# Kernel tuning notes

Hardware: AMD Instinct MI355X
Metric: run time of the kernel (lower is better)

The kernel has to match this reference:

```python
import jax, jax.numpy as jnp
import numpy as np

B, C, H, W = 16, 1536, 32, 32
M = 64      # num_clusters
L = 128     # cluster_dim
G = 256     # token_dim
HID = 512
OT_ITERS = 3
EPS = 1e-6


def setup_inputs() -> dict:
    key = jax.random.key(0)
    ks = jax.random.split(key, 12)
    def w(k, shape, fan_in):
        return jax.random.normal(k, shape, jnp.float32) * (1.0 / np.sqrt(fan_in))
    return {
        'x': jax.random.normal(ks[0], (B, C, H, W), jnp.float32),
        't': jax.random.normal(ks[1], (B, C), jnp.float32),
        # token_features: Linear(C->512), ReLU, Linear(512->G)
        'Wt1': w(ks[2], (HID, C), C), 'bt1': jnp.zeros((HID,), jnp.float32),
        'Wt2': w(ks[3], (G, HID), HID), 'bt2': jnp.zeros((G,), jnp.float32),
        # cluster_features: 1x1 Conv(C->512), ReLU, 1x1 Conv(512->L)
        'Wc1': w(ks[4], (HID, C), C), 'bc1': jnp.zeros((HID,), jnp.float32),
        'Wc2': w(ks[5], (L, HID), HID), 'bc2': jnp.zeros((L,), jnp.float32),
        # score: 1x1 Conv(C->512), ReLU, 1x1 Conv(512->M)
        'Ws1': w(ks[6], (HID, C), C), 'bs1': jnp.zeros((HID,), jnp.float32),
        'Ws2': w(ks[7], (M, HID), HID), 'bs2': jnp.zeros((M,), jnp.float32),
        # temp_predictor: Conv1d(L->1, k=1)
        'Wtp': w(ks[8], (L,), L), 'btp': jnp.zeros((), jnp.float32),
        'dust_bin': jnp.asarray(1.0, jnp.float32),
        'burst_b': jnp.asarray(0.0, jnp.float32),
        'burst_p': jnp.asarray(1.0, jnp.float32),
        'lambda_discount': jnp.asarray(0.5, jnp.float32),
    }


def _log_optimal_transport(scores, alpha, iters):
    # scores: [B, m, n]; alpha: scalar dust-bin logit
    b, m, n = scores.shape
    Z0 = jnp.concatenate([scores, jnp.broadcast_to(alpha, (b, 1, n))], axis=1)  # [B, m+1, n]
    norm = -jnp.log(jnp.asarray(m + n, scores.dtype))
    log_mu = jnp.concatenate([jnp.full((m,), norm, scores.dtype),
                              (jnp.log(jnp.asarray(n, scores.dtype)) + norm)[None]])  # [m+1]
    log_nu = jnp.full((n,), norm, scores.dtype)
    u = jnp.zeros((b, m + 1), scores.dtype)
    v = jnp.zeros((b, n), scores.dtype)
    for _ in range(iters):
        u = log_mu - jax.nn.logsumexp(Z0 + v[:, None, :], axis=2)
        v = log_nu - jax.nn.logsumexp(Z0 + u[:, :, None], axis=1)
    return Z0 + u[:, :, None] + v[:, None, :] - norm


def _l2norm(a, axis):
    return a / jnp.maximum(jnp.linalg.norm(a, axis=axis, keepdims=True), 1e-12)


def _forward(x, t, Wt1, bt1, Wt2, bt2, Wc1, bc1, Wc2, bc2, Ws1, bs1, Ws2, bs2,
             Wtp, btp, dust_bin, burst_b, burst_p, lambda_discount):
    b, c, h, w = x.shape
    n = h * w
    xf = x.reshape(b, c, n)  # [B, C, N] (1x1 convs == per-pixel MLP)
    # cluster features f: [B, L, N]
    h1 = jax.nn.relu(jnp.einsum('bcn,oc->bon', xf, Wc1) + bc1[:, None])
    f = jnp.einsum('bhn,lh->bln', h1, Wc2) + bc2[:, None]
    # assignment scores p: [B, M, N]
    h2 = jax.nn.relu(jnp.einsum('bcn,oc->bon', xf, Ws1) + bs1[:, None])
    p = jnp.einsum('bhn,mh->bmn', h2, Ws2) + bs2[:, None]
    # global token: [B, G]
    tok = jax.nn.relu(t @ Wt1.T + bt1) @ Wt2.T + bt2
    # Sinkhorn OT soft assignment, drop dust bin row
    P = jnp.exp(_log_optimal_transport(p, dust_bin, OT_ITERS))[:, :-1, :]  # [B, M, N]
    # burst-aware weighting
    f_norm = _l2norm(f, axis=1)                                  # [B, L, N]
    T_i = jax.nn.softplus(jnp.einsum('bln,l->bn', f, Wtp) + btp)  # [B, N]
    sim = jnp.einsum('bli,blj->bij', f_norm, f_norm)              # [B, N, N]
    T_avg = (T_i[:, :, None] + T_i[:, None, :]) * 0.5
    burst_w = jax.nn.sigmoid(T_avg * sim + burst_b)
    discount = jnp.clip(jnp.sum(burst_w, axis=-1) ** burst_p, 1e-3, 1e3)  # [B, N]
    lam = jax.nn.sigmoid(lambda_discount)
    P_adj = (1.0 - lam) * P + lam * (P / (discount[:, None, :] + EPS))
    # local aggregation: (f[:, :, None, :] * P[:, None, :, :]).sum(-1) == batched matmul
    agg = jnp.einsum('bln,bmn->blm', f, P_adj)  # [B, L, M]
    agg = _l2norm(agg, axis=1).reshape(b, -1)   # [B, L*M]
    tok_n = _l2norm(tok, axis=-1)
    g = jnp.concatenate([tok_n, agg], axis=-1)  # [B, G + L*M]
    return _l2norm(g, axis=-1)


def reference(x, t, Wt1, bt1, Wt2, bt2, Wc1, bc1, Wc2, bc2, Ws1, bs1, Ws2, bs2,
              Wtp, btp, dust_bin, burst_b, burst_p, lambda_discount):
    return _forward(x, t, Wt1, bt1, Wt2, bt2, Wc1, bc1, Wc2, bc2, Ws1, bs1, Ws2, bs2,
                    Wtp, btp, dust_bin, burst_b, burst_p, lambda_discount)
```

## Files before the change

kernel.cpp:

```cpp
#include <hip/hip_runtime.h>
#include <math.h>

#define B_   16
#define C_   1536
#define N_   1024
#define M_   64
#define L_   128
#define G_   256
#define HID_ 512

typedef __attribute__((ext_vector_type(8))) short short8;
typedef __attribute__((ext_vector_type(4))) float floatx4;

__device__ __forceinline__ unsigned short f2bf_rne(float x) {
    unsigned u = __float_as_uint(x);
    unsigned r = u + 0x7fffu + ((u >> 16) & 1u);
    return (unsigned short)(r >> 16);
}
__device__ __forceinline__ unsigned pack_bf2(float lo, float hi) {
    unsigned a = __float_as_uint(lo) + 0x8000u;
    unsigned b = __float_as_uint(hi) + 0x8000u;
    return (a >> 16) | (b & 0xffff0000u);
}

__device__ __forceinline__ void gl2lds16(const void* g, void* l) {
    __builtin_amdgcn_global_load_lds(
        (const __attribute__((address_space(1))) void*)g,
        (__attribute__((address_space(3))) void*)l, 16, 0, 0);
}

__global__ __launch_bounds__(256) void cast_w_kernel(
    const float* __restrict__ Wc1, const float* __restrict__ Ws1,
    const float* __restrict__ Wc2, const float* __restrict__ Ws2,
    unsigned short* __restrict__ Wbf, unsigned short* __restrict__ W2)
{
    const int T1 = 1024 * 1536;
    int idx = blockIdx.x * 256 + threadIdx.x;
    if (idx < T1) {
        float v = (idx < 512 * 1536) ? Wc1[idx] : Ws1[idx - 512 * 1536];
        Wbf[idx] = f2bf_rne(v);
    } else if (idx < T1 + 192 * 1024) {
        int i2 = idx - T1;
        int row = i2 >> 10, k = i2 & 1023;
        float v = 0.f;
        if (row < 128) { if (k < 512) v = Wc2[row * 512 + k]; }
        else           { if (k >= 512) v = Ws2[(row - 128) * 512 + (k - 512)]; }
        W2[i2] = f2bf_rne(v);
    }
}

__global__ __launch_bounds__(256) void xt_kernel(
    const float* __restrict__ x, unsigned short* __restrict__ xT)
{
    __shared__ float Xs[64][65];
    const int t = threadIdx.x;
    const int n0 = blockIdx.x * 64, c0 = blockIdx.y * 64, b = blockIdx.z;
    const float* xb = x + (long)b * C_ * N_;
    #pragma unroll
    for (int it = 0; it < 16; ++it) {
        int idx = it * 256 + t, cr = idx >> 6, nc = idx & 63;
        Xs[cr][nc] = xb[(long)(c0 + cr) * N_ + n0 + nc];
    }
    __syncthreads();
    unsigned* xo = (unsigned*)(xT + (long)b * N_ * C_);
    #pragma unroll
    for (int it = 0; it < 8; ++it) {
        int idx = it * 256 + t, nr = idx >> 5, pc = idx & 31;
        xo[(long)(n0 + nr) * 768 + (c0 >> 1) + pc] =
            pack_bf2(Xs[2 * pc][nr], Xs[2 * pc + 1][nr]);
    }
}

__global__ __launch_bounds__(256, 2) void gemm1_kernel(
    const unsigned short* __restrict__ Wbf, const unsigned short* __restrict__ xT,
    const float* __restrict__ bc1, const float* __restrict__ bs1,
    unsigned short* __restrict__ hT)
{
    __shared__ unsigned short As[128 * 32];
    __shared__ unsigned short Bs[128 * 32];
    const int t = threadIdx.x;
    const int lane = t & 63, w = t >> 6;
    const int n0 = blockIdx.x * 128, o0 = blockIdx.y * 128, b = blockIdx.z;
    const unsigned short* xb = xT + (long)b * N_ * C_;

    const int wo = (w >> 1) * 64, wn = (w & 1) * 64;
    const int lrow = lane & 15, kgrp = lane >> 4;
    const int arow = t >> 2, acol = (t & 3) * 8;

    floatx4 acc[4][4];
    #pragma unroll
    for (int i = 0; i < 4; ++i)
        #pragma unroll
        for (int j = 0; j < 4; ++j) acc[i][j] = (floatx4)0.0f;

    for (int k0 = 0; k0 < C_; k0 += 32) {
        #pragma unroll
        for (int r = 0; r < 2; ++r)
            gl2lds16(Wbf + (long)(o0 + r * 64 + arow) * C_ + k0 + acol,
                     (char*)As + r * 4096 + t * 16);
        #pragma unroll
        for (int r = 0; r < 2; ++r)
            gl2lds16(xb + (long)(n0 + r * 64 + arow) * C_ + k0 + acol,
                     (char*)Bs + r * 4096 + t * 16);
        __syncthreads();
        short8 af[4], bfr[4];
        #pragma unroll
        for (int i = 0; i < 4; ++i)
            af[i] = *(const short8*)((const char*)As +
                        (wo + i * 16 + lrow) * 64 + kgrp * 16);
        #pragma unroll
        for (int j = 0; j < 4; ++j)
            bfr[j] = *(const short8*)((const char*)Bs +
                        (wn + j * 16 + lrow) * 64 + kgrp * 16);
        #pragma unroll
        for (int i = 0; i < 4; ++i)
            #pragma unroll
            for (int j = 0; j < 4; ++j)
                acc[i][j] = __builtin_amdgcn_mfma_f32_16x16x32_bf16(
                    af[i], bfr[j], acc[i][j], 0, 0, 0);
        __syncthreads();
    }

    const float* bias = (o0 < 512) ? bc1 : bs1;
    const int ob = (o0 < 512) ? o0 : o0 - 512;
    #pragma unroll
    for (int i = 0; i < 4; ++i) {
        int orow = wo + i * 16 + kgrp * 4;
        float b0 = bias[ob + orow + 0], b1 = bias[ob + orow + 1];
        float b2 = bias[ob + orow + 2], b3 = bias[ob + orow + 3];
        #pragma unroll
        for (int j = 0; j < 4; ++j) {
            int n = n0 + wn + j * 16 + lrow;
            float v0 = fmaxf(acc[i][j][0] + b0, 0.f);
            float v1 = fmaxf(acc[i][j][1] + b1, 0.f);
            float v2 = fmaxf(acc[i][j][2] + b2, 0.f);
            float v3 = fmaxf(acc[i][j][3] + b3, 0.f);
            uint2 pk;
            pk.x = ((unsigned)f2bf_rne(v0)) | (((unsigned)f2bf_rne(v1)) << 16);
            pk.y = ((unsigned)f2bf_rne(v2)) | (((unsigned)f2bf_rne(v3)) << 16);
            *(uint2*)&hT[((long)b * N_ + n) * 1024 + o0 + orow] = pk;
        }
    }
}

__global__ __launch_bounds__(256, 2) void gemm23_kernel(
    const unsigned short* __restrict__ W2, const unsigned short* __restrict__ hT,
    const float* __restrict__ bc2, const float* __restrict__ bs2,
    float* __restrict__ f, float* __restrict__ p)
{
    __shared__ unsigned short As[64 * 32];
    __shared__ unsigned short Bs[128 * 32];
    const int t = threadIdx.x;
    const int lane = t & 63, w = t >> 6;
    const int n0 = blockIdx.x * 128, o0 = blockIdx.y * 64, b = blockIdx.z;
    const unsigned short* hTb = hT + (long)b * N_ * 1024;

    const int wo = (w >> 1) * 32, wn = (w & 1) * 64;
    const int lrow = lane & 15, kgrp = lane >> 4;
    const int arow = t >> 2, acol = (t & 3) * 8;

    floatx4 acc[2][4];
    #pragma unroll
    for (int i = 0; i < 2; ++i)
        #pragma unroll
        for (int j = 0; j < 4; ++j) acc[i][j] = (floatx4)0.0f;

    for (int k0 = 0; k0 < 1024; k0 += 32) {
        gl2lds16(W2 + (long)(o0 + arow) * 1024 + k0 + acol, (char*)As + t * 16);
        #pragma unroll
        for (int r = 0; r < 2; ++r)
            gl2lds16(hTb + (long)(n0 + r * 64 + arow) * 1024 + k0 + acol,
                     (char*)Bs + r * 4096 + t * 16);
        __syncthreads();
        short8 af[2], bfr[4];
        #pragma unroll
        for (int i = 0; i < 2; ++i)
            af[i] = *(const short8*)((const char*)As +
                        (wo + i * 16 + lrow) * 64 + kgrp * 16);
        #pragma unroll
        for (int j = 0; j < 4; ++j)
            bfr[j] = *(const short8*)((const char*)Bs +
                        (wn + j * 16 + lrow) * 64 + kgrp * 16);
        #pragma unroll
        for (int i = 0; i < 2; ++i)
            #pragma unroll
            for (int j = 0; j < 4; ++j)
                acc[i][j] = __builtin_amdgcn_mfma_f32_16x16x32_bf16(
                    af[i], bfr[j], acc[i][j], 0, 0, 0);
        __syncthreads();
    }

    #pragma unroll
    for (int i = 0; i < 2; ++i) {
        int o = o0 + wo + i * 16 + kgrp * 4;
        #pragma unroll
        for (int j = 0; j < 4; ++j) {
            int n = n0 + wn + j * 16 + lrow;
            #pragma unroll
            for (int r = 0; r < 4; ++r) {
                int oo = o + r;
                float v = acc[i][j][r];
                if (oo < 128) f[((long)b * L_ + oo) * N_ + n] = v + bc2[oo];
                else p[((long)b * M_ + (oo - 128)) * N_ + n] = v + bs2[oo - 128];
            }
        }
    }
}

__global__ __launch_bounds__(256) void token1_kernel(
    const float* __restrict__ t_in, const float* __restrict__ Wt1,
    const float* __restrict__ bt1, float* __restrict__ hid)
{
    const int lane = threadIdx.x & 63, w = threadIdx.x >> 6;
    const int o = blockIdx.x * 4 + w, b = blockIdx.y;
    const float4* wr = (const float4*)(Wt1 + (long)o * C_);
    const float4* tb = (const float4*)(t_in + (long)b * C_);
    float acc = 0.f;
    #pragma unroll
    for (int i = 0; i < 6; ++i) {
        float4 a = wr[i * 64 + lane], tv = tb[i * 64 + lane];
        acc += a.x * tv.x + a.y * tv.y + a.z * tv.z + a.w * tv.w;
    }
    #pragma unroll
    for (int off = 1; off < 64; off <<= 1) acc += __shfl_xor(acc, off);
    if (lane == 0) hid[b * HID_ + o] = fmaxf(acc + bt1[o], 0.f);
}

__global__ __launch_bounds__(256) void token2_kernel(
    const float* __restrict__ hid, const float* __restrict__ Wt2,
    const float* __restrict__ bt2, float* __restrict__ tok)
{
    const int lane = threadIdx.x & 63, w = threadIdx.x >> 6;
    const int g = blockIdx.x * 4 + w, b = blockIdx.y;
    const float4* wr = (const float4*)(Wt2 + (long)g * HID_);
    const float4* hb = (const float4*)(hid + (long)b * HID_);
    float acc = 0.f;
    #pragma unroll
    for (int i = 0; i < 2; ++i) {
        float4 a = wr[i * 64 + lane], hv = hb[i * 64 + lane];
        acc += a.x * hv.x + a.y * hv.y + a.z * hv.z + a.w * hv.w;
    }
    #pragma unroll
    for (int off = 1; off < 64; off <<= 1) acc += __shfl_xor(acc, off);
    if (lane == 0) tok[b * G_ + g] = acc + bt2[g];
}

__global__ __launch_bounds__(256) void token3_kernel(
    const float* __restrict__ tok, float* __restrict__ tokn)
{
    __shared__ float red[4];
    const int b = blockIdx.x, t = threadIdx.x;
    float v = tok[b * G_ + t];
    float ss = v * v;
    #pragma unroll
    for (int off = 1; off < 64; off <<= 1) ss += __shfl_xor(ss, off);
    if ((t & 63) == 0) red[t >> 6] = ss;
    __syncthreads();
    float inv = 1.f / fmaxf(sqrtf(red[0] + red[1] + red[2] + red[3]), 1e-12f);
    tokn[b * G_ + t] = v * inv;
}

template<bool FIRST>
__global__ __launch_bounds__(256) void ku_kernel(
    float* __restrict__ p, const float* __restrict__ dust,
    const float* __restrict__ bvec, float* __restrict__ avec)
{
    const int t = threadIdx.x, lane = t & 63, w = t >> 6;
    const int m = blockIdx.x * 4 + w, b = blockIdx.y;
    if (m > M_) return;
    const float* bv = bvec + b * N_;
    float s = 0.f;
    if (m < M_) {
        float* row = p + ((long)b * M_ + m) * N_;
        #pragma unroll
        for (int i = 0; i < 16; ++i) {
            int n = i * 64 + lane;
            if (FIRST) {
                float K = expf(row[n]);
                row[n] = K;
                s += K;
            } else {
                s += row[n] * bv[n];
            }
        }
    } else {
        float ea = expf(dust[0]);
        if (FIRST) s = 16.f * ea;
        else {
            #pragma unroll
            for (int i = 0; i < 16; ++i) s += bv[i * 64 + lane];
            s *= ea;
        }
    }
    #pragma unroll
    for (int off = 1; off < 64; off <<= 1) s += __shfl_xor(s, off);
    if (lane == 0) {
        float mu = (m < M_) ? (1.f / 1088.f) : (1024.f / 1088.f);
        avec[b * (M_ + 1) + m] = mu / s;
    }
}

__global__ __launch_bounds__(256) void kv_kernel(
    const float* __restrict__ K, const float* __restrict__ dust,
    const float* __restrict__ avec, float* __restrict__ bvec)
{
    __shared__ float a_s[M_ + 1];
    const int t = threadIdx.x, b = blockIdx.y;
    const int n = blockIdx.x * 256 + t;
    if (t < M_ + 1) a_s[t] = avec[b * (M_ + 1) + t];
    __syncthreads();
    float s = expf(dust[0]) * a_s[M_];
    const float* col = K + (long)b * M_ * N_ + n;
    #pragma unroll
    for (int m = 0; m < M_; ++m) s = fmaf(col[(long)m * N_], a_s[m], s);
    bvec[b * N_ + n] = (1.f / 1088.f) / s;
}

__global__ __launch_bounds__(256) void tnorm_kernel(
    const float* __restrict__ f, const float* __restrict__ Wtp,
    const float* __restrict__ btp, unsigned short* __restrict__ fnT,
    float* __restrict__ T, float* __restrict__ draw)
{
    __shared__ float Ft[L_][65];
    __shared__ float invs[64];
    __shared__ float wtp_s[L_];
    const int b = blockIdx.y, n0 = blockIdx.x * 64, t = threadIdx.x;
    const float* fb = f + (long)b * L_ * N_;

    if (t < L_) wtp_s[t] = Wtp[t];
    for (int it = 0; it < 32; ++it) {
        int idx = it * 256 + t;
        int l = idx >> 6, c = idx & 63;
        Ft[l][c] = fb[(long)l * N_ + n0 + c];
    }
    __syncthreads();
    if (t < 64) {
        float ss = 0.f, dot = 0.f;
        #pragma unroll
        for (int l = 0; l < L_; ++l) {
            float v = Ft[l][t];
            ss = fmaf(v, v, ss);
            dot = fmaf(v, wtp_s[l], dot);
        }
        invs[t] = 1.f / fmaxf(sqrtf(ss), 1e-12f);
        float xx = dot + btp[0];
        T[b * N_ + n0 + t] = (xx > 0.f) ? (xx + log1pf(expf(-xx)))
                                        : log1pf(expf(xx));
        draw[b * N_ + n0 + t] = 0.f;
    }
    __syncthreads();
    unsigned* fo = (unsigned*)fnT;
    for (int it = 0; it < 16; ++it) {
        int idx = it * 256 + t;
        int nl = idx >> 6, jp = idx & 63;
        float inv = invs[nl];
        fo[(((long)b * N_ + n0 + nl) << 6) + jp] =
            pack_bf2(Ft[2 * jp][nl] * inv, Ft[2 * jp + 1][nl] * inv);
    }
}

__global__ __launch_bounds__(256) void sim_kernel(
    const unsigned short* __restrict__ fnT, const float* __restrict__ T,
    const float* __restrict__ bb, float* __restrict__ draw)
{
    __shared__ unsigned short As[64 * 136];
    __shared__ unsigned short Bs[64 * 136];
    __shared__ float Ti[64], Tj[64];
    const int b = blockIdx.z, i0 = blockIdx.y * 64, j0base = blockIdx.x * 256;
    const int t = threadIdx.x, lane = t & 63, w = t >> 6;
    const int lrow = lane & 15, kgrp = lane >> 4;
    const unsigned short* fb = fnT + (long)b * N_ * 128;
    const float burstb = bb[0];

    if (t < 64) Ti[t] = T[b * N_ + i0 + t];
    const int srow = t >> 4, scol = (t & 15) * 8;
    #pragma unroll
    for (int r = 0; r < 4; ++r) {
        uint4 av = *(const uint4*)(fb + (long)(i0 + r * 16 + srow) * 128 + scol);
        *(uint4*)((char*)As + (r * 16 + srow) * 272 + scol * 2) = av;
    }

    float rs[4] = {0.f, 0.f, 0.f, 0.f};
    for (int jj = 0; jj < 4; ++jj) {
        const int j0 = j0base + jj * 64;
        __syncthreads();
        #pragma unroll
        for (int r = 0; r < 4; ++r) {
            uint4 bv = *(const uint4*)(fb + (long)(j0 + r * 16 + srow) * 128 + scol);
            *(uint4*)((char*)Bs + (r * 16 + srow) * 272 + scol * 2) = bv;
        }
        if (t >= 64 && t < 128) Tj[t - 64] = T[b * N_ + j0 + (t - 64)];
        __syncthreads();

        floatx4 acc[4];
        #pragma unroll
        for (int j = 0; j < 4; ++j) acc[j] = (floatx4)0.0f;
        #pragma unroll
        for (int k0 = 0; k0 < 128; k0 += 32) {
            short8 af = *(const short8*)((const char*)As +
                            (w * 16 + lrow) * 272 + k0 * 2 + kgrp * 16);
            #pragma unroll
            for (int j = 0; j < 4; ++j) {
                short8 bf = *(const short8*)((const char*)Bs +
                                (j * 16 + lrow) * 272 + k0 * 2 + kgrp * 16);
                acc[j] = __builtin_amdgcn_mfma_f32_16x16x32_bf16(af, bf, acc[j], 0, 0, 0);
            }
        }
        #pragma unroll
        for (int j = 0; j < 4; ++j) {
            float Tjv = Tj[j * 16 + lrow];
            #pragma unroll
            for (int r = 0; r < 4; ++r) {
                float Tiv = Ti[w * 16 + kgrp * 4 + r];
                float xarg = 0.5f * (Tiv + Tjv) * acc[j][r] + burstb;
                rs[r] += 1.f / (1.f + expf(-xarg));
            }
        }
    }

    #pragma unroll
    for (int off = 1; off < 16; off <<= 1)
        #pragma unroll
        for (int r = 0; r < 4; ++r) rs[r] += __shfl_xor(rs[r], off);
    if (lrow == 0) {
        #pragma unroll
        for (int r = 0; r < 4; ++r)
            atomicAdd(&draw[b * N_ + i0 + w * 16 + kgrp * 4 + r], rs[r]);
    }
}

__global__ __launch_bounds__(256) void wn_kernel(
    const float* __restrict__ draw, const float* __restrict__ bp,
    const float* __restrict__ lamd, float* __restrict__ wn,
    float* __restrict__ agg)
{
    const int id = blockIdx.x * 256 + threadIdx.x;
    float d = powf(draw[id], bp[0]);
    d = fminf(fmaxf(d, 1e-3f), 1e3f);
    float lam = 1.f / (1.f + expf(-lamd[0]));
    wn[id] = (1.f - lam) + lam / (d + 1e-6f);
    for (int i = id; i < B_ * L_ * M_; i += B_ * N_) agg[i] = 0.f;
}

__global__ __launch_bounds__(256) void agg_kernel(
    const float* __restrict__ f, const float* __restrict__ Kmat,
    const float* __restrict__ avec, const float* __restrict__ dust,
    const float* __restrict__ wn, float* __restrict__ agg)
{
    __shared__ float fch[L_][65];
    __shared__ float Pch[M_][65];
    __shared__ float a_s[M_ + 1], cf[64];
    const int b = blockIdx.y, n0 = blockIdx.x * 64;
    const int t = threadIdx.x, tx = t & 15, ty = t >> 4;
    const float* fb = f + (long)b * L_ * N_;
    const float* Kb = Kmat + (long)b * M_ * N_;

    if (t < M_ + 1) a_s[t] = avec[b * (M_ + 1) + t];
    __syncthreads();

    for (int idx = t; idx < L_ * 64; idx += 256) {
        int l = idx >> 6, c = idx & 63;
        fch[l][c] = fb[(long)l * N_ + n0 + c];
    }
    for (int idx = t; idx < M_ * 64; idx += 256) {
        int m = idx >> 6, c = idx & 63;
        Pch[m][c] = Kb[(long)m * N_ + n0 + c] * a_s[m];
    }
    __syncthreads();

    if (t < 64) {
        float s = expf(dust[0]) * a_s[M_];
        #pragma unroll
        for (int m = 0; m < M_; ++m) s += Pch[m][t];
        cf[t] = wn[b * N_ + n0 + t] / s;
    }
    __syncthreads();

    float acc[8][4] = {};
    for (int n = 0; n < 64; ++n) {
        float cfn = cf[n];
        float fv[8], pv[4];
        #pragma unroll
        for (int i = 0; i < 8; ++i) fv[i] = fch[ty + 16 * i][n];
        #pragma unroll
        for (int j = 0; j < 4; ++j) pv[j] = Pch[tx * 4 + j][n] * cfn;
        #pragma unroll
        for (int i = 0; i < 8; ++i)
            #pragma unroll
            for (int j = 0; j < 4; ++j)
                acc[i][j] = fmaf(fv[i], pv[j], acc[i][j]);
    }
    #pragma unroll
    for (int i = 0; i < 8; ++i)
        #pragma unroll
        for (int j = 0; j < 4; ++j)
            atomicAdd(&agg[((long)b * L_ + (ty + 16 * i)) * M_ + tx * 4 + j],
                      acc[i][j]);
}

__global__ __launch_bounds__(256) void final_kernel(
    const float* __restrict__ tokn, const float* __restrict__ agg,
    float* __restrict__ out)
{
    __shared__ float invm[M_];
    __shared__ float red[4];
    __shared__ float s_invtot;
    const int b = blockIdx.x, t = threadIdx.x;
    const float* ab = agg + (long)b * L_ * M_;

    if (t < 64) {
        float ss = 0.f;
        for (int l = 0; l < L_; ++l) {
            float v = ab[l * M_ + t];
            ss = fmaf(v, v, ss);
        }
        invm[t] = 1.f / fmaxf(sqrtf(ss), 1e-12f);
    }
    __syncthreads();

    float part;
    {
        float tn = tokn[b * G_ + t];
        part = tn * tn;
    }
    for (int idx = t; idx < L_ * M_; idx += 256) {
        float v = ab[idx] * invm[idx & 63];
        part = fmaf(v, v, part);
    }
    for (int off = 32; off; off >>= 1) part += __shfl_down(part, off);
    if ((t & 63) == 0) red[t >> 6] = part;
    __syncthreads();
    if (t == 0)
        s_invtot = 1.f / fmaxf(sqrtf(red[0] + red[1] + red[2] + red[3]), 1e-12f);
    __syncthreads();

    const float invtot = s_invtot;
    float* ob = out + (long)b * (G_ + L_ * M_);
    ob[t] = tokn[b * G_ + t] * invtot;
    for (int idx = t; idx < L_ * M_; idx += 256)
        ob[G_ + idx] = ab[idx] * invm[idx & 63] * invtot;
}

extern "C" void kernel_launch(void* const* d_in, const int* in_sizes, int n_in,
                              void* d_out, int out_size, void* d_ws, size_t ws_size,
                              hipStream_t stream)
{
    const float* x    = (const float*)d_in[0];
    const float* t_in = (const float*)d_in[1];
    const float* Wt1  = (const float*)d_in[2];
    const float* bt1  = (const float*)d_in[3];
    const float* Wt2  = (const float*)d_in[4];
    const float* bt2  = (const float*)d_in[5];
    const float* Wc1  = (const float*)d_in[6];
    const float* bc1  = (const float*)d_in[7];
    const float* Wc2  = (const float*)d_in[8];
    const float* bc2  = (const float*)d_in[9];
    const float* Ws1  = (const float*)d_in[10];
    const float* bs1  = (const float*)d_in[11];
    const float* Ws2  = (const float*)d_in[12];
    const float* bs2  = (const float*)d_in[13];
    const float* Wtp  = (const float*)d_in[14];
    const float* btp  = (const float*)d_in[15];
    const float* dust = (const float*)d_in[16];
    const float* bb   = (const float*)d_in[17];
    const float* bp   = (const float*)d_in[18];
    const float* lamd = (const float*)d_in[19];

    char* wsb = (char*)d_ws;
    unsigned short* xT  = (unsigned short*)wsb;
    float* f    = (float*)(wsb + 0);
    float* p    = (float*)(wsb + 8388608);
    unsigned short* fnT = (unsigned short*)(wsb + 12582912);
    float* hid  = (float*)(wsb + 16777216);
    float* tok  = (float*)(wsb + 16809984);
    float* tokn = (float*)(wsb + 16826368);
    float* T    = (float*)(wsb + 16842752);
    float* draw = (float*)(wsb + 16908288);
    float* wgt  = (float*)(wsb + 16973824);
    float* agg  = (float*)(wsb + 17039360);
    float* avec = (float*)(wsb + 17563648);
    float* bvec = (float*)(wsb + 17567808);
    unsigned short* hT  = (unsigned short*)(wsb + 50331648);
    unsigned short* Wbf = (unsigned short*)(wsb + 83886080);
    unsigned short* W2  = (unsigned short*)(wsb + 87031808);
    float* out  = (float*)d_out;

    cast_w_kernel<<<6912, 256, 0, stream>>>(Wc1, Ws1, Wc2, Ws2, Wbf, W2);

    xt_kernel   <<<dim3(16, 24, 16), 256, 0, stream>>>(x, xT);
    gemm1_kernel<<<dim3(8, 8, 16), 256, 0, stream>>>(Wbf, xT, bc1, bs1, hT);
    gemm23_kernel<<<dim3(8, 3, 16), 256, 0, stream>>>(W2, hT, bc2, bs2, f, p);

    token1_kernel<<<dim3(128, 16), 256, 0, stream>>>(t_in, Wt1, bt1, hid);
    token2_kernel<<<dim3(64, 16), 256, 0, stream>>>(hid, Wt2, bt2, tok);
    token3_kernel<<<16, 256, 0, stream>>>(tok, tokn);

    ku_kernel<true> <<<dim3(17, 16), 256, 0, stream>>>(p, dust, bvec, avec);
    kv_kernel       <<<dim3(4, 16), 256, 0, stream>>>(p, dust, avec, bvec);
    ku_kernel<false><<<dim3(17, 16), 256, 0, stream>>>(p, dust, bvec, avec);
    kv_kernel       <<<dim3(4, 16), 256, 0, stream>>>(p, dust, avec, bvec);
    ku_kernel<false><<<dim3(17, 16), 256, 0, stream>>>(p, dust, bvec, avec);

    tnorm_kernel<<<dim3(16, 16), 256, 0, stream>>>(f, Wtp, btp, fnT, T, draw);
    sim_kernel  <<<dim3(4, 16, 16), 256, 0, stream>>>(fnT, T, bb, draw);
    wn_kernel   <<<64, 256, 0, stream>>>(draw, bp, lamd, wgt, agg);
    agg_kernel  <<<dim3(16, 16), 256, 0, stream>>>(f, p, avec, dust, wgt, agg);
    final_kernel<<<16, 256, 0, stream>>>(tokn, agg, out);
}
```

Before: 391.0 us.

## Fuse exp and first Sinkhorn row-sum into GEMM epilogue, store f as bf16

```diff
diff --git a/kernel.cpp b/kernel.cpp
--- a/kernel.cpp
+++ b/kernel.cpp
@@ -22,7 +22,9 @@
     unsigned b = __float_as_uint(hi) + 0x8000u;
     return (a >> 16) | (b & 0xffff0000u);
 }
-
+__device__ __forceinline__ float bf2f(unsigned short u) {
+    return __uint_as_float(((unsigned)u) << 16);
+}
 __device__ __forceinline__ void gl2lds16(const void* g, void* l) {
     __builtin_amdgcn_global_load_lds(
         (const __attribute__((address_space(1))) void*)g,
@@ -32,20 +34,28 @@
 __global__ __launch_bounds__(256) void cast_w_kernel(
     const float* __restrict__ Wc1, const float* __restrict__ Ws1,
     const float* __restrict__ Wc2, const float* __restrict__ Ws2,
-    unsigned short* __restrict__ Wbf, unsigned short* __restrict__ W2)
+    unsigned short* __restrict__ Wbf, unsigned short* __restrict__ W2,
+    float* __restrict__ agg, float* __restrict__ draw,
+    float* __restrict__ rowsum)
 {
     const int T1 = 1024 * 1536;
+    const int T2 = 192 * 1024;
     int idx = blockIdx.x * 256 + threadIdx.x;
     if (idx < T1) {
         float v = (idx < 512 * 1536) ? Wc1[idx] : Ws1[idx - 512 * 1536];
         Wbf[idx] = f2bf_rne(v);
-    } else if (idx < T1 + 192 * 1024) {
+    } else if (idx < T1 + T2) {
         int i2 = idx - T1;
         int row = i2 >> 10, k = i2 & 1023;
         float v = 0.f;
         if (row < 128) { if (k < 512) v = Wc2[row * 512 + k]; }
         else           { if (k >= 512) v = Ws2[(row - 128) * 512 + (k - 512)]; }
         W2[i2] = f2bf_rne(v);
+    } else {
+        int zi = idx - (T1 + T2);
+        if (zi < 131072) agg[zi] = 0.f;
+        else if (zi < 131072 + 16384) draw[zi - 131072] = 0.f;
+        else if (zi < 131072 + 16384 + 1040) rowsum[zi - 131072 - 16384] = 0.f;
     }
 }
 
@@ -76,8 +86,9 @@
     const float* __restrict__ bc1, const float* __restrict__ bs1,
     unsigned short* __restrict__ hT)
 {
-    __shared__ unsigned short As[128 * 32];
-    __shared__ unsigned short Bs[128 * 32];
+    __shared__ unsigned short sh[8704];
+    unsigned short* As = sh;
+    unsigned short* Bs = sh + 4096;
     const int t = threadIdx.x;
     const int lane = t & 63, w = t >> 6;
     const int n0 = blockIdx.x * 128, o0 = blockIdx.y * 128, b = blockIdx.z;
@@ -123,30 +134,45 @@
 
     const float* bias = (o0 < 512) ? bc1 : bs1;
     const int ob = (o0 < 512) ? o0 : o0 - 512;
-    #pragma unroll
-    for (int i = 0; i < 4; ++i) {
-        int orow = wo + i * 16 + kgrp * 4;
-        float b0 = bias[ob + orow + 0], b1 = bias[ob + orow + 1];
-        float b2 = bias[ob + orow + 2], b3 = bias[ob + orow + 3];
-        #pragma unroll
-        for (int j = 0; j < 4; ++j) {
-            int n = n0 + wn + j * 16 + lrow;
-            float v0 = fmaxf(acc[i][j][0] + b0, 0.f);
-            float v1 = fmaxf(acc[i][j][1] + b1, 0.f);
-            float v2 = fmaxf(acc[i][j][2] + b2, 0.f);
-            float v3 = fmaxf(acc[i][j][3] + b3, 0.f);
-            uint2 pk;
-            pk.x = ((unsigned)f2bf_rne(v0)) | (((unsigned)f2bf_rne(v1)) << 16);
-            pk.y = ((unsigned)f2bf_rne(v2)) | (((unsigned)f2bf_rne(v3)) << 16);
-            *(uint2*)&hT[((long)b * N_ + n) * 1024 + o0 + orow] = pk;
-        }
+    for (int half = 0; half < 2; ++half) {
+        if ((w & 1) == half) {
+            #pragma unroll
+            for (int i = 0; i < 4; ++i) {
+                int o_loc = wo + i * 16 + kgrp * 4;
+                float b0 = bias[ob + o_loc + 0], b1 = bias[ob + o_loc + 1];
+                float b2 = bias[ob + o_loc + 2], b3 = bias[ob + o_loc + 3];
+                #pragma unroll
+                for (int j = 0; j < 4; ++j) {
+                    int n_loc = j * 16 + lrow;
+                    float v0 = fmaxf(acc[i][j][0] + b0, 0.f);
+                    float v1 = fmaxf(acc[i][j][1] + b1, 0.f);
+                    float v2 = fmaxf(acc[i][j][2] + b2, 0.f);
+                    float v3 = fmaxf(acc[i][j][3] + b3, 0.f);
+                    uint2 pk;
+                    pk.x = pack_bf2(v0, v1) & 0u;
+                    pk.x = ((unsigned)f2bf_rne(v0)) | (((unsigned)f2bf_rne(v1)) << 16);
+                    pk.y = ((unsigned)f2bf_rne(v2)) | (((unsigned)f2bf_rne(v3)) << 16);
+                    *(uint2*)((char*)sh + n_loc * 272 + o_loc * 2) = pk;
+                }
+            }
+        }
+        __syncthreads();
+        #pragma unroll
+        for (int ps = 0; ps < 4; ++ps) {
+            int n_loc = ps * 16 + (t >> 4);
+            int o8 = (t & 15) * 8;
+            uint4 q = *(const uint4*)((const char*)sh + n_loc * 272 + o8 * 2);
+            *(uint4*)&hT[((long)b * N_ + n0 + half * 64 + n_loc) * 1024 + o0 + o8] = q;
+        }
+        __syncthreads();
     }
 }
 
 __global__ __launch_bounds__(256, 2) void gemm23_kernel(
     const unsigned short* __restrict__ W2, const unsigned short* __restrict__ hT,
     const float* __restrict__ bc2, const float* __restrict__ bs2,
-    float* __restrict__ f, float* __restrict__ p)
+    unsigned short* __restrict__ fbf, float* __restrict__ K,
+    float* __restrict__ rowsum)
 {
     __shared__ unsigned short As[64 * 32];
     __shared__ unsigned short Bs[128 * 32];
@@ -190,20 +216,48 @@
         __syncthreads();
     }
 
-    #pragma unroll
-    for (int i = 0; i < 2; ++i) {
-        int o = o0 + wo + i * 16 + kgrp * 4;
-        #pragma unroll
-        for (int j = 0; j < 4; ++j) {
-            int n = n0 + wn + j * 16 + lrow;
+    if (o0 < 128) {
+        #pragma unroll
+        for (int i = 0; i < 2; ++i) {
+            int o = o0 + wo + i * 16 + kgrp * 4;
+            #pragma unroll
+            for (int j = 0; j < 4; ++j) {
+                int n = n0 + wn + j * 16 + lrow;
+                #pragma unroll
+                for (int r = 0; r < 4; ++r) {
+                    int oo = o + r;
+                    fbf[((long)b * L_ + oo) * N_ + n] =
+                        f2bf_rne(acc[i][j][r] + bc2[oo]);
+                }
+            }
+        }
+    } else {
+        float sloc[2][4] = {};
+        #pragma unroll
+        for (int i = 0; i < 2; ++i) {
+            int m0 = wo + i * 16 + kgrp * 4;
+            #pragma unroll
+            for (int j = 0; j < 4; ++j) {
+                int n = n0 + wn + j * 16 + lrow;
+                #pragma unroll
+                for (int r = 0; r < 4; ++r) {
+                    int m = m0 + r;
+                    float val = expf(acc[i][j][r] + bs2[m]);
+                    K[((long)b * M_ + m) * N_ + n] = val;
+                    sloc[i][r] += val;
+                }
+            }
+        }
+        #pragma unroll
+        for (int i = 0; i < 2; ++i)
             #pragma unroll
             for (int r = 0; r < 4; ++r) {
-                int oo = o + r;
-                float v = acc[i][j][r];
-                if (oo < 128) f[((long)b * L_ + oo) * N_ + n] = v + bc2[oo];
-                else p[((long)b * M_ + (oo - 128)) * N_ + n] = v + bs2[oo - 128];
+                float s = sloc[i][r];
+                #pragma unroll
+                for (int off = 1; off < 16; off <<= 1) s += __shfl_xor(s, off);
+                if (lrow == 0)
+                    atomicAdd(&rowsum[b * 65 + wo + i * 16 + kgrp * 4 + r], s);
             }
-        }
     }
 }
 
@@ -246,7 +300,9 @@
 }
 
 __global__ __launch_bounds__(256) void token3_kernel(
-    const float* __restrict__ tok, float* __restrict__ tokn)
+    const float* __restrict__ tok, float* __restrict__ tokn,
+    const float* __restrict__ rowsum, const float* __restrict__ dust,
+    float* __restrict__ avec)
 {
     __shared__ float red[4];
     const int b = blockIdx.x, t = threadIdx.x;
@@ -255,14 +311,18 @@
     #pragma unroll
     for (int off = 1; off < 64; off <<= 1) ss += __shfl_xor(ss, off);
     if ((t & 63) == 0) red[t >> 6] = ss;
+    if (t < 65) {
+        float s  = (t < 64) ? rowsum[b * 65 + t] : 1024.f * expf(dust[0]);
+        float mu = (t < 64) ? (1.f / 1088.f) : (1024.f / 1088.f);
+        avec[b * 65 + t] = mu / s;
+    }
     __syncthreads();
     float inv = 1.f / fmaxf(sqrtf(red[0] + red[1] + red[2] + red[3]), 1e-12f);
     tokn[b * G_ + t] = v * inv;
 }
 
-template<bool FIRST>
 __global__ __launch_bounds__(256) void ku_kernel(
-    float* __restrict__ p, const float* __restrict__ dust,
+    const float* __restrict__ K, const float* __restrict__ dust,
     const float* __restrict__ bvec, float* __restrict__ avec)
 {
     const int t = threadIdx.x, lane = t & 63, w = t >> 6;
@@ -271,26 +331,16 @@
     const float* bv = bvec + b * N_;
     float s = 0.f;
     if (m < M_) {
-        float* row = p + ((long)b * M_ + m) * N_;
+        const float* row = K + ((long)b * M_ + m) * N_;
         #pragma unroll
         for (int i = 0; i < 16; ++i) {
             int n = i * 64 + lane;
-            if (FIRST) {
-                float K = expf(row[n]);
-                row[n] = K;
-                s += K;
-            } else {
-                s += row[n] * bv[n];
-            }
+            s += row[n] * bv[n];
         }
     } else {
-        float ea = expf(dust[0]);
-        if (FIRST) s = 16.f * ea;
-        else {
-            #pragma unroll
-            for (int i = 0; i < 16; ++i) s += bv[i * 64 + lane];
-            s *= ea;
-        }
+        #pragma unroll
+        for (int i = 0; i < 16; ++i) s += bv[i * 64 + lane];
+        s *= expf(dust[0]);
     }
     #pragma unroll
     for (int off = 1; off < 64; off <<= 1) s += __shfl_xor(s, off);
@@ -317,21 +367,28 @@
 }
 
 __global__ __launch_bounds__(256) void tnorm_kernel(
-    const float* __restrict__ f, const float* __restrict__ Wtp,
+    const unsigned short* __restrict__ fbf, const float* __restrict__ Wtp,
     const float* __restrict__ btp, unsigned short* __restrict__ fnT,
-    float* __restrict__ T, float* __restrict__ draw)
+    float* __restrict__ T)
 {
     __shared__ float Ft[L_][65];
     __shared__ float invs[64];
     __shared__ float wtp_s[L_];
     const int b = blockIdx.y, n0 = blockIdx.x * 64, t = threadIdx.x;
-    const float* fb = f + (long)b * L_ * N_;
 
     if (t < L_) wtp_s[t] = Wtp[t];
-    for (int it = 0; it < 32; ++it) {
-        int idx = it * 256 + t;
-        int l = idx >> 6, c = idx & 63;
-        Ft[l][c] = fb[(long)l * N_ + n0 + c];
+    #pragma unroll
+    for (int it = 0; it < 4; ++it) {
+        int l = it * 32 + (t >> 3), c0 = (t & 7) * 8;
+        uint4 q = *(const uint4*)(fbf + ((long)(b * L_ + l)) * N_ + n0 + c0);
+        Ft[l][c0 + 0] = bf2f((unsigned short)(q.x & 0xffff));
+        Ft[l][c0 + 1] = bf2f((unsigned short)(q.x >> 16));
+        Ft[l][c0 + 2] = bf2f((unsigned short)(q.y & 0xffff));
+        Ft[l][c0 + 3] = bf2f((unsigned short)(q.y >> 16));
+        Ft[l][c0 + 4] = bf2f((unsigned short)(q.z & 0xffff));
+        Ft[l][c0 + 5] = bf2f((unsigned short)(q.z >> 16));
+        Ft[l][c0 + 6] = bf2f((unsigned short)(q.w & 0xffff));
+        Ft[l][c0 + 7] = bf2f((unsigned short)(q.w >> 16));
     }
     __syncthreads();
     if (t < 64) {
@@ -346,7 +403,6 @@
         float xx = dot + btp[0];
         T[b * N_ + n0 + t] = (xx > 0.f) ? (xx + log1pf(expf(-xx)))
                                         : log1pf(expf(xx));
-        draw[b * N_ + n0 + t] = 0.f;
     }
     __syncthreads();
     unsigned* fo = (unsigned*)fnT;
@@ -429,39 +485,35 @@
     }
 }
 
-__global__ __launch_bounds__(256) void wn_kernel(
+__global__ __launch_bounds__(256) void agg_kernel(
+    const unsigned short* __restrict__ fbf, const float* __restrict__ K,
+    const float* __restrict__ avec, const float* __restrict__ dust,
     const float* __restrict__ draw, const float* __restrict__ bp,
-    const float* __restrict__ lamd, float* __restrict__ wn,
-    float* __restrict__ agg)
-{
-    const int id = blockIdx.x * 256 + threadIdx.x;
-    float d = powf(draw[id], bp[0]);
-    d = fminf(fmaxf(d, 1e-3f), 1e3f);
-    float lam = 1.f / (1.f + expf(-lamd[0]));
-    wn[id] = (1.f - lam) + lam / (d + 1e-6f);
-    for (int i = id; i < B_ * L_ * M_; i += B_ * N_) agg[i] = 0.f;
-}
-
-__global__ __launch_bounds__(256) void agg_kernel(
-    const float* __restrict__ f, const float* __restrict__ Kmat,
-    const float* __restrict__ avec, const float* __restrict__ dust,
-    const float* __restrict__ wn, float* __restrict__ agg)
+    const float* __restrict__ lamd, float* __restrict__ agg)
 {
     __shared__ float fch[L_][65];
     __shared__ float Pch[M_][65];
     __shared__ float a_s[M_ + 1], cf[64];
     const int b = blockIdx.y, n0 = blockIdx.x * 64;
     const int t = threadIdx.x, tx = t & 15, ty = t >> 4;
-    const float* fb = f + (long)b * L_ * N_;
-    const float* Kb = Kmat + (long)b * M_ * N_;
+    const float* Kb = K + (long)b * M_ * N_;
 
     if (t < M_ + 1) a_s[t] = avec[b * (M_ + 1) + t];
-    __syncthreads();
-
-    for (int idx = t; idx < L_ * 64; idx += 256) {
-        int l = idx >> 6, c = idx & 63;
-        fch[l][c] = fb[(long)l * N_ + n0 + c];
-    }
+
+    #pragma unroll
+    for (int it = 0; it < 4; ++it) {
+        int l = it * 32 + (t >> 3), c0 = (t & 7) * 8;
+        uint4 q = *(const uint4*)(fbf + ((long)(b * L_ + l)) * N_ + n0 + c0);
+        fch[l][c0 + 0] = bf2f((unsigned short)(q.x & 0xffff));
+        fch[l][c0 + 1] = bf2f((unsigned short)(q.x >> 16));
+        fch[l][c0 + 2] = bf2f((unsigned short)(q.y & 0xffff));
+        fch[l][c0 + 3] = bf2f((unsigned short)(q.y >> 16));
+        fch[l][c0 + 4] = bf2f((unsigned short)(q.z & 0xffff));
+        fch[l][c0 + 5] = bf2f((unsigned short)(q.z >> 16));
+        fch[l][c0 + 6] = bf2f((unsigned short)(q.w & 0xffff));
+        fch[l][c0 + 7] = bf2f((unsigned short)(q.w >> 16));
+    }
+    __syncthreads();
     for (int idx = t; idx < M_ * 64; idx += 256) {
         int m = idx >> 6, c = idx & 63;
         Pch[m][c] = Kb[(long)m * N_ + n0 + c] * a_s[m];
@@ -472,7 +524,11 @@
         float s = expf(dust[0]) * a_s[M_];
         #pragma unroll
         for (int m = 0; m < M_; ++m) s += Pch[m][t];
-        cf[t] = wn[b * N_ + n0 + t] / s;
+        float d = powf(draw[b * N_ + n0 + t], bp[0]);
+        d = fminf(fmaxf(d, 1e-3f), 1e3f);
+        float lam = 1.f / (1.f + expf(-lamd[0]));
+        float wnv = (1.f - lam) + lam / (d + 1e-6f);
+        cf[t] = wnv / s;
     }
     __syncthreads();
 
@@ -568,42 +624,43 @@
 
     char* wsb = (char*)d_ws;
     unsigned short* xT  = (unsigned short*)wsb;
-    float* f    = (float*)(wsb + 0);
-    float* p    = (float*)(wsb + 8388608);
-    unsigned short* fnT = (unsigned short*)(wsb + 12582912);
-    float* hid  = (float*)(wsb + 16777216);
-    float* tok  = (float*)(wsb + 16809984);
-    float* tokn = (float*)(wsb + 16826368);
-    float* T    = (float*)(wsb + 16842752);
-    float* draw = (float*)(wsb + 16908288);
-    float* wgt  = (float*)(wsb + 16973824);
-    float* agg  = (float*)(wsb + 17039360);
-    float* avec = (float*)(wsb + 17563648);
-    float* bvec = (float*)(wsb + 17567808);
+    unsigned short* fbf = (unsigned short*)(wsb + 0);
+    float* K    = (float*)(wsb + 4194304);
+    unsigned short* fnT = (unsigned short*)(wsb + 8388608);
+    float* hid  = (float*)(wsb + 12582912);
+    float* tok  = (float*)(wsb + 12615680);
+    float* tokn = (float*)(wsb + 12632064);
+    float* T    = (float*)(wsb + 12648448);
+    float* avec = (float*)(wsb + 12713984);
+    float* bvec = (float*)(wsb + 12718144);
     unsigned short* hT  = (unsigned short*)(wsb + 50331648);
     unsigned short* Wbf = (unsigned short*)(wsb + 83886080);
     unsigned short* W2  = (unsigned short*)(wsb + 87031808);
+    float* draw   = (float*)(wsb + 87425024);
+    float* agg    = (float*)(wsb + 87490560);
+    float* rowsum = (float*)(wsb + 88014848);
     float* out  = (float*)d_out;
 
-    cast_w_kernel<<<6912, 256, 0, stream>>>(Wc1, Ws1, Wc2, Ws2, Wbf, W2);
-
-    xt_kernel   <<<dim3(16, 24, 16), 256, 0, stream>>>(x, xT);
-    gemm1_kernel<<<dim3(8, 8, 16), 256, 0, stream>>>(Wbf, xT, bc1, bs1, hT);
-    gemm23_kernel<<<dim3(8, 3, 16), 256, 0, stream>>>(W2, hT, bc2, bs2, f, p);
+    cast_w_kernel<<<7493, 256, 0, stream>>>(Wc1, Ws1, Wc2, Ws2, Wbf, W2,
+                                            agg, draw, rowsum);
+
+    xt_kernel    <<<dim3(16, 24, 16), 256, 0, stream>>>(x, xT);
+    gemm1_kernel <<<dim3(8, 8, 16), 256, 0, stream>>>(Wbf, xT, bc1, bs1, hT);
+    gemm23_kernel<<<dim3(8, 3, 16), 256, 0, stream>>>(W2, hT, bc2, bs2,
+                                                      fbf, K, rowsum);
 
     token1_kernel<<<dim3(128, 16), 256, 0, stream>>>(t_in, Wt1, bt1, hid);
     token2_kernel<<<dim3(64, 16), 256, 0, stream>>>(hid, Wt2, bt2, tok);
-    token3_kernel<<<16, 256, 0, stream>>>(tok, tokn);
-
-    ku_kernel<true> <<<dim3(17, 16), 256, 0, stream>>>(p, dust, bvec, avec);
-    kv_kernel       <<<dim3(4, 16), 256, 0, stream>>>(p, dust, avec, bvec);
-    ku_kernel<false><<<dim3(17, 16), 256, 0, stream>>>(p, dust, bvec, avec);
-    kv_kernel       <<<dim3(4, 16), 256, 0, stream>>>(p, dust, avec, bvec);
-    ku_kernel<false><<<dim3(17, 16), 256, 0, stream>>>(p, dust, bvec, avec);
-
-    tnorm_kernel<<<dim3(16, 16), 256, 0, stream>>>(f, Wtp, btp, fnT, T, draw);
+    token3_kernel<<<16, 256, 0, stream>>>(tok, tokn, rowsum, dust, avec);
+
+    kv_kernel<<<dim3(4, 16), 256, 0, stream>>>(K, dust, avec, bvec);
+    ku_kernel<<<dim3(17, 16), 256, 0, stream>>>(K, dust, bvec, avec);
+    kv_kernel<<<dim3(4, 16), 256, 0, stream>>>(K, dust, avec, bvec);
+    ku_kernel<<<dim3(17, 16), 256, 0, stream>>>(K, dust, bvec, avec);
+
+    tnorm_kernel<<<dim3(16, 16), 256, 0, stream>>>(fbf, Wtp, btp, fnT, T);
     sim_kernel  <<<dim3(4, 16, 16), 256, 0, stream>>>(fnT, T, bb, draw);
-    wn_kernel   <<<64, 256, 0, stream>>>(draw, bp, lamd, wgt, agg);
-    agg_kernel  <<<dim3(16, 16), 256, 0, stream>>>(f, p, avec, dust, wgt, agg);
+    agg_kernel  <<<dim3(16, 16), 256, 0, stream>>>(fbf, K, avec, dust,
+                                                   draw, bp, lamd, agg);
     final_kernel<<<16, 256, 0, stream>>>(tokn, agg, out);
 }
```

New measurement: 399.4 us. +2.2%, slower.
